# Performance work log

Measured on AMD Instinct MI355X. Metric: run time of the kernel, lower is better.

Reference implementation:

```python
import jax, jax.numpy as jnp
import numpy as np

EPS = 1e-5

def _conv3x3(x, w):
    # x: [B,C,H,W], w: [O,I,3,3], stride 1, padding 1
    return jax.lax.conv_general_dilated(
        x, w, window_strides=(1, 1), padding=((1, 1), (1, 1)),
        dimension_numbers=('NCHW', 'OIHW', 'NCHW'))

def _bn(x, gamma, beta, mean, var):
    inv = gamma / jnp.sqrt(var + EPS)
    return x * inv[None, :, None, None] + (beta - mean * inv)[None, :, None, None]

def setup_inputs() -> dict:
    key = jax.random.key(0)
    ks = jax.random.split(key, 6)
    B, C, H, W, E = 32, 64, 112, 112, 10
    x = jax.random.normal(ks[0], (B, C, H, W), dtype=jnp.float32)
    w1 = jax.random.normal(ks[1], (E, C, C, 3, 3), dtype=jnp.float32) * 0.05
    w2 = jax.random.normal(ks[2], (E, C, C, 3, 3), dtype=jnp.float32) * 0.05
    alpha = jax.random.uniform(ks[3], (E,), dtype=jnp.float32)
    return {
        'x': x, 'w1': w1, 'w2': w2, 'alpha': alpha,
        'bn1_gamma': jnp.ones((C,), jnp.float32),
        'bn1_beta': jnp.zeros((C,), jnp.float32),
        'bn1_mean': jnp.zeros((C,), jnp.float32),
        'bn1_var': jax.random.uniform(ks[4], (C,), jnp.float32) + 0.5,
        'bn2_gamma': jnp.ones((C,), jnp.float32),
        'bn2_beta': jnp.zeros((C,), jnp.float32),
        'bn2_mean': jnp.zeros((C,), jnp.float32),
        'bn2_var': jax.random.uniform(ks[5], (C,), jnp.float32) + 0.5,
    }

def reference(x, w1, w2, alpha,
              bn1_gamma, bn1_beta, bn1_mean, bn1_var,
              bn2_gamma, bn2_beta, bn2_mean, bn2_var):
    # Convolution is linear in its weights, so sum_i alpha[i] * conv(x, w_i)
    # == conv(x, sum_i alpha[i] * w_i): pre-combine experts into one kernel.
    w1_eff = jnp.einsum('e,eoihw->oihw', alpha, w1)
    w2_eff = jnp.einsum('e,eoihw->oihw', alpha, w2)
    out = _conv3x3(x, w1_eff)
    out = jax.nn.relu(_bn(out, bn1_gamma, bn1_beta, bn1_mean, bn1_var))
    out = _conv3x3(out, w2_eff)
    out = _bn(out, bn2_gamma, bn2_beta, bn2_mean, bn2_var)
    return jax.nn.relu(out + x)
```

## Files before the change

kernel.cpp:

```cpp
#include <hip/hip_runtime.h>


typedef __bf16 bf16x8 __attribute__((ext_vector_type(8)));
typedef float f32x4 __attribute__((ext_vector_type(4)));
typedef unsigned short u16;
typedef u16 u16x8 __attribute__((ext_vector_type(8)));

#define NH 112
#define NW 112
#define PH 114
#define PW 114
#define PROWB (PW * 128)
#define BUFB 23040
#define NTILES 3136

#define WAITVM(n) asm volatile("s_waitcnt vmcnt(" #n ")" ::: "memory")
#define SCHEDB __builtin_amdgcn_sched_barrier(0)

__device__ __forceinline__ u16 f2b(float f) {
  unsigned u = __builtin_bit_cast(unsigned, f);
  u += 0x7FFFu + ((u >> 16) & 1u);
  return (u16)(u >> 16);
}
__device__ __forceinline__ float b2f(u16 b) {
  unsigned u = ((unsigned)b) << 16;
  return __builtin_bit_cast(float, u);
}

__device__ __forceinline__ void gl_lds16(const void* g, void* l) {
  __builtin_amdgcn_global_load_lds(
      (const __attribute__((address_space(1))) unsigned int*)g,
      (__attribute__((address_space(3))) unsigned int*)l, 16, 0, 0);
}

__global__ void border_zero(u16* __restrict__ a, u16* __restrict__ bbuf) {
  int idx = blockIdx.x * 256 + threadIdx.x;
  if (idx >= 231424) return;
  int c8 = idx & 7;
  int t = idx >> 3;
  int buf = t >= 14464;
  t -= buf * 14464;
  int img = t / 452, e = t % 452;
  int h, w;
  if (e < 114) { h = 0; w = e; }
  else if (e < 228) { h = 113; w = e - 114; }
  else if (e < 340) { h = e - 227; w = 0; }
  else { h = e - 339; w = 113; }
  u16* base = buf ? bbuf : a;
  u16x8 z = {0, 0, 0, 0, 0, 0, 0, 0};
  *reinterpret_cast<u16x8*>(base + (((long)img * PH + h) * PW + w) * 64 + c8 * 8) = z;
}

__global__ __launch_bounds__(256) void transform_kernel(const float* __restrict__ x,
                                                        u16* __restrict__ xpad) {
  __shared__ alignas(16) u16 t[7168];
  int tid = threadIdx.x, bid = blockIdx.x;
  int b = bid / NH, h = bid % NH;
  const float* src = x + (long)b * 64 * 12544 + h * NW;
  f32x4 v[7];
#pragma unroll
  for (int it = 0; it < 7; ++it) {
    int fid = it * 256 + tid;
    int c = fid / 28, wq = fid % 28;
    v[it] = *reinterpret_cast<const f32x4*>(src + c * 12544 + wq * 4);
  }
#pragma unroll
  for (int it = 0; it < 7; ++it) {
    int fid = it * 256 + tid;
    int c = fid / 28, wq = fid % 28;
    int key = (wq & 7) << 4;
#pragma unroll
    for (int j = 0; j < 4; ++j) {
      int px = wq * 4 + j;
      *reinterpret_cast<u16*>((char*)t + px * 128 + ((c * 2) ^ key)) = f2b(v[it][j]);
    }
  }
  __syncthreads();
  int hp = h + 1;
  u16* rowb = xpad + (((long)b * PH + hp) * PW) * 64;
#pragma unroll
  for (int it = 0; it < 4; ++it) {
    int cidx = it * 256 + tid;
    if (cidx < 896) {
      int c8 = cidx & 7, px = cidx >> 3;
      int lchunk = c8 ^ ((px >> 2) & 7);
      u16x8 vv = *reinterpret_cast<const u16x8*>((const char*)t + px * 128 + lchunk * 16);
      int wp = px + 1;
      int gkey = (2 * hp + wp) & 7;
      *reinterpret_cast<u16x8*>(rowb + (long)wp * 64 + ((c8 ^ gkey) * 8)) = vv;
    }
  }
}

__global__ void prep_kernel(
    const float* __restrict__ w1, const float* __restrict__ w2,
    const float* __restrict__ alpha,
    const float* __restrict__ g1, const float* __restrict__ b1,
    const float* __restrict__ m1, const float* __restrict__ v1,
    const float* __restrict__ g2, const float* __restrict__ b2,
    const float* __restrict__ m2, const float* __restrict__ v2,
    u16* __restrict__ weff1, u16* __restrict__ weff2, float* __restrict__ bnc) {
  int idx = blockIdx.x * 256 + threadIdx.x;
  if (idx < 36864) {
    int i = idx & 63;
    int o = (idx >> 6) & 63;
    int kpos = idx >> 12;
    int base = (o * 64 + i) * 9 + kpos;
    float a1 = 0.f, a2 = 0.f;
#pragma unroll
    for (int e = 0; e < 10; ++e) {
      float al = alpha[e];
      a1 += al * w1[e * 36864 + base];
      a2 += al * w2[e * 36864 + base];
    }
    weff1[idx] = f2b(a1);
    weff2[idx] = f2b(a2);
  }
  if (blockIdx.x == 0 && threadIdx.x < 64) {
    int c = threadIdx.x;
    float i1 = g1[c] * rsqrtf(v1[c] + 1e-5f);
    float i2 = g2[c] * rsqrtf(v2[c] + 1e-5f);
    bnc[c] = i1;
    bnc[64 + c] = b1[c] - m1[c] * i1;
    bnc[128 + c] = i2;
    bnc[192 + c] = b2[c] - m2[c] * i2;
  }
}

__global__ __launch_bounds__(256, 2) void conv_p0_kernel(
    const u16* __restrict__ xin, const u16* __restrict__ weff,
    const float* __restrict__ bnc, u16* __restrict__ ypad) {
  __shared__ alignas(64) char smem[2 * BUFB];

  int tid = threadIdx.x, lane = tid & 63, wv = tid >> 6;
  int ol = lane & 15, kg = (lane >> 4) & 3;
  const int o = wv * 16 + ol;

  float inv = bnc[o];
  float bias = bnc[64 + o];

  bf16x8 wf[3][3][2];
#pragma unroll
  for (int kh = 0; kh < 3; ++kh)
#pragma unroll
    for (int kw = 0; kw < 3; ++kw)
#pragma unroll
      for (int ks = 0; ks < 2; ++ks)
        wf[kh][kw][ks] = __builtin_bit_cast(
            bf16x8, *reinterpret_cast<const u16x8*>(
                        weff + (((kh * 3 + kw) * 64 + o) * 64 + ks * 32 + kg * 8)));
  asm volatile("s_waitcnt vmcnt(0)" ::: "memory");
  SCHEDB;

  const int sb = (blockIdx.x & 7) * 64 + (blockIdx.x >> 3);
  const int n = (NTILES - sb + 511) >> 9;

  auto stage = [&](int tt, int boff) {
    int b = tt / 98;
    int r = tt % 98;
    int h0 = (r / 7) * 8, w0 = (r % 7) * 16;
    const char* src = (const char*)(xin + (((long)b * PH + h0) * PW + w0) * 64);
#pragma unroll
    for (int k = 0; k < 6; ++k) {
      int i = wv + k * 4;
      if (i < 23) {
        int cb = i * 64 + lane;
        if (cb < 1440) {
          int row = cb / 144, rem = cb % 144;
          gl_lds16(src + (long)row * PROWB + rem * 16, smem + boff + cb * 16);
        }
      }
    }
  };

  stage(sb, 0);
  asm volatile("" ::: "memory");
  stage(sb + 512, BUFB);
  asm volatile("" ::: "memory");
  if (wv < 3) WAITVM(6);
  else        WAITVM(5);
  SCHEDB;

  for (int j = 0; j < n; ++j) {
    const int boff = (j & 1) * BUFB;
    const int tt = sb + (j << 9);
    const int b = tt / 98;
    const int r = tt % 98;
    const int th0 = (r / 7) * 8, tw0 = (r % 7) * 16;

    __builtin_amdgcn_s_barrier();
    SCHEDB;

    f32x4 acc[8];
#pragma unroll
    for (int mf = 0; mf < 8; ++mf) acc[mf] = f32x4{0.f, 0.f, 0.f, 0.f};

#pragma unroll
    for (int kw = 0; kw < 3; ++kw)
#pragma unroll
      for (int ks = 0; ks < 2; ++ks) {
        const int col = ol + kw;
        const int sb8 = (ks << 2) | kg;
        bf16x8 a[4];
#pragma unroll
        for (int u = 0; u < 3; ++u) {
          int slot = sb8 ^ ((2 * u + col) & 7);
          a[u] = *reinterpret_cast<const bf16x8*>(smem + boff + (u * 18 + col) * 128 +
                                                  slot * 16);
        }
#pragma unroll
        for (int mf = 0; mf < 8; ++mf) {
          if (mf < 7) {
            int rr = mf + 3;
            int slot = sb8 ^ ((2 * rr + col) & 7);
            a[(mf + 3) & 3] = *reinterpret_cast<const bf16x8*>(
                smem + boff + (rr * 18 + col) * 128 + slot * 16);
          }
          acc[mf] = __builtin_amdgcn_mfma_f32_16x16x32_bf16(a[mf & 3], wf[0][kw][ks],
                                                            acc[mf], 0, 0, 0);
          acc[mf] = __builtin_amdgcn_mfma_f32_16x16x32_bf16(a[(mf + 1) & 3], wf[1][kw][ks],
                                                            acc[mf], 0, 0, 0);
          acc[mf] = __builtin_amdgcn_mfma_f32_16x16x32_bf16(a[(mf + 2) & 3], wf[2][kw][ks],
                                                            acc[mf], 0, 0, 0);
        }
      }

    SCHEDB;
    __builtin_amdgcn_s_barrier();
    SCHEDB;
    u16* ys = reinterpret_cast<u16*>(smem + boff);
#pragma unroll
    for (int mf = 0; mf < 8; ++mf)
#pragma unroll
      for (int rg = 0; rg < 4; ++rg) {
        int p = mf * 16 + kg * 4 + rg;
        ys[p * 72 + o] = f2b(fmaxf(acc[mf][rg] * inv + bias, 0.f));
      }
    asm volatile("s_waitcnt lgkmcnt(0)" ::: "memory");
    SCHEDB;
    __builtin_amdgcn_s_barrier();
    SCHEDB;
#pragma unroll
    for (int it = 0; it < 4; ++it) {
      int cidx = it * 256 + tid;
      int c8 = cidx & 7, p = cidx >> 3;
      int hp = th0 + (p >> 4) + 1, wp = tw0 + (p & 15) + 1;
      int gkey = (2 * hp + wp) & 7;
      *reinterpret_cast<u16x8*>(ypad + (((long)b * PH + hp) * PW + wp) * 64 +
                                ((c8 ^ gkey) * 8)) =
          *reinterpret_cast<const u16x8*>(ys + p * 72 + c8 * 8);
    }

    if (j + 1 < n) {
      SCHEDB;
      __builtin_amdgcn_s_barrier();
      SCHEDB;
      if (j + 2 < n) {
        stage(sb + ((j + 2) << 9), boff);
        if (wv < 3) WAITVM(6);
        else        WAITVM(5);
      } else {
        WAITVM(0);
      }
      SCHEDB;
    }
  }
}

template <int RESID>
__global__ __launch_bounds__(256, 2) void conv_p1_kernel(
    const u16* __restrict__ yin, const float* __restrict__ x,
    const u16* __restrict__ xres, const u16* __restrict__ weff,
    const float* __restrict__ bnc, float* __restrict__ out) {
  constexpr int BUF = RESID ? (BUFB + 16384) : BUFB;
  __shared__ alignas(64) char smem[2 * BUF];

  int tid = threadIdx.x, lane = tid & 63, wv = tid >> 6;
  int ol = lane & 15, kg = (lane >> 4) & 3;
  const int o = wv * 16 + ol;

  float inv = bnc[128 + o];
  float bias = bnc[192 + o];

  bf16x8 wf[3][3][2];
#pragma unroll
  for (int kh = 0; kh < 3; ++kh)
#pragma unroll
    for (int kw = 0; kw < 3; ++kw)
#pragma unroll
      for (int ks = 0; ks < 2; ++ks)
        wf[kh][kw][ks] = __builtin_bit_cast(
            bf16x8, *reinterpret_cast<const u16x8*>(
                        weff + (((kh * 3 + kw) * 64 + o) * 64 + ks * 32 + kg * 8)));
  asm volatile("s_waitcnt vmcnt(0)" ::: "memory");
  SCHEDB;

  const int sb = (blockIdx.x & 7) * 64 + (blockIdx.x >> 3);
  const int n = (NTILES - sb + 511) >> 9;

  auto stage = [&](int tt, int boff) {
    int b = tt / 98;
    int r = tt % 98;
    int h0 = (r / 7) * 8, w0 = (r % 7) * 16;
    const char* src = (const char*)(yin + (((long)b * PH + h0) * PW + w0) * 64);
#pragma unroll
    for (int k = 0; k < 6; ++k) {
      int i = wv + k * 4;
      if (i < 23) {
        int cb = i * 64 + lane;
        if (cb < 1440) {
          int row = cb / 144, rem = cb % 144;
          gl_lds16(src + (long)row * PROWB + rem * 16, smem + boff + cb * 16);
        }
      }
    }
    if constexpr (RESID) {
#pragma unroll
      for (int k = 0; k < 4; ++k) {
        int i = wv + k * 4;
        int cr = i * 64 + lane;
        int rp = cr >> 7, rem = cr & 127;
        gl_lds16((const char*)xres + (((long)b * PH + h0 + 1 + rp) * PW + w0 + 1) * 128 +
                     rem * 16,
                 smem + boff + BUFB + cr * 16);
      }
    }
  };
  auto gateS = [&] {
    if constexpr (RESID) {
      if (wv < 3) WAITVM(10); else WAITVM(9);
    } else {
      if (wv < 3) WAITVM(6); else WAITVM(5);
    }
  };

  stage(sb, 0);
  asm volatile("" ::: "memory");
  stage(sb + 512, BUF);
  asm volatile("" ::: "memory");
  gateS();
  SCHEDB;

  for (int j = 0; j < n; ++j) {
    const int boff = (j & 1) * BUF;
    const int tt = sb + (j << 9);
    const int b = tt / 98;
    const int r = tt % 98;
    const int th0 = (r / 7) * 8, tw0 = (r % 7) * 16;

    __builtin_amdgcn_s_barrier();
    SCHEDB;

    f32x4 acc[8];
#pragma unroll
    for (int mf = 0; mf < 8; ++mf) acc[mf] = f32x4{0.f, 0.f, 0.f, 0.f};

#pragma unroll
    for (int kw = 0; kw < 3; ++kw)
#pragma unroll
      for (int ks = 0; ks < 2; ++ks) {
        const int col = ol + kw;
        const int sb8 = (ks << 2) | kg;
        bf16x8 a[4];
#pragma unroll
        for (int u = 0; u < 3; ++u) {
          int slot = sb8 ^ ((2 * u + col) & 7);
          a[u] = *reinterpret_cast<const bf16x8*>(smem + boff + (u * 18 + col) * 128 +
                                                  slot * 16);
        }
#pragma unroll
        for (int mf = 0; mf < 8; ++mf) {
          if (mf < 7) {
            int rr = mf + 3;
            int slot = sb8 ^ ((2 * rr + col) & 7);
            a[(mf + 3) & 3] = *reinterpret_cast<const bf16x8*>(
                smem + boff + (rr * 18 + col) * 128 + slot * 16);
          }
          acc[mf] = __builtin_amdgcn_mfma_f32_16x16x32_bf16(a[mf & 3], wf[0][kw][ks],
                                                            acc[mf], 0, 0, 0);
          acc[mf] = __builtin_amdgcn_mfma_f32_16x16x32_bf16(a[(mf + 1) & 3], wf[1][kw][ks],
                                                            acc[mf], 0, 0, 0);
          acc[mf] = __builtin_amdgcn_mfma_f32_16x16x32_bf16(a[(mf + 2) & 3], wf[2][kw][ks],
                                                            acc[mf], 0, 0, 0);
        }
      }

    if constexpr (RESID) {
#pragma unroll
      for (int mf = 0; mf < 8; ++mf) {
        int h = th0 + mf, hp = h + 1;
        f32x4 vv;
#pragma unroll
        for (int rg = 0; rg < 4; ++rg) {
          int wq = kg * 4 + rg, wp = tw0 + wq + 1;
          int key = (2 * hp + wp) & 7;
          u16 bv = *reinterpret_cast<const u16*>(
              smem + boff + BUFB + (mf * 16 + wq) * 128 + (((o >> 3) ^ key) * 16) +
              (o & 7) * 2);
          vv[rg] = fmaxf(acc[mf][rg] * inv + bias + b2f(bv), 0.f);
        }
        *reinterpret_cast<f32x4*>(out + (((b * 64 + o) * NH + h) * NW + tw0 + kg * 4)) =
            vv;
      }
    } else {
#pragma unroll
      for (int half = 0; half < 2; ++half) {
        f32x4 xr[4];
#pragma unroll
        for (int m = 0; m < 4; ++m) {
          int h = th0 + half * 4 + m;
          xr[m] = *reinterpret_cast<const f32x4*>(
              x + (((b * 64 + o) * NH + h) * NW + tw0 + kg * 4));
        }
#pragma unroll
        for (int m = 0; m < 4; ++m) {
          int mf = half * 4 + m;
          int h = th0 + mf;
          f32x4 vv;
#pragma unroll
          for (int rg = 0; rg < 4; ++rg)
            vv[rg] = fmaxf(acc[mf][rg] * inv + bias + xr[m][rg], 0.f);
          *reinterpret_cast<f32x4*>(out + (((b * 64 + o) * NH + h) * NW + tw0 + kg * 4)) =
              vv;
        }
      }
    }

    if (j + 1 < n) {
      SCHEDB;
      __builtin_amdgcn_s_barrier();
      SCHEDB;
      if (j + 2 < n) {
        stage(sb + ((j + 2) << 9), boff);
        gateS();
      } else {
        WAITVM(0);
      }
      SCHEDB;
    }
  }
}

extern "C" void kernel_launch(void* const* d_in, const int* in_sizes, int n_in,
                              void* d_out, int out_size, void* d_ws, size_t ws_size,
                              hipStream_t stream) {
  const float* x = (const float*)d_in[0];
  const float* w1 = (const float*)d_in[1];
  const float* w2 = (const float*)d_in[2];
  const float* alpha = (const float*)d_in[3];
  const float* g1 = (const float*)d_in[4];
  const float* b1 = (const float*)d_in[5];
  const float* m1 = (const float*)d_in[6];
  const float* v1 = (const float*)d_in[7];
  const float* g2 = (const float*)d_in[8];
  const float* b2 = (const float*)d_in[9];
  const float* m2 = (const float*)d_in[10];
  const float* v2 = (const float*)d_in[11];
  float* out = (float*)d_out;

  char* ws = (char*)d_ws;
  u16* weff1 = (u16*)ws;
  u16* weff2 = (u16*)(ws + 73728);
  float* bnc = (float*)(ws + 147456);
  u16* y1pad = (u16*)(ws + 148480);
  const size_t PADB = 53231616ull;
  bool big = ws_size >= 148480ull + 2ull * PADB;
  u16* xpad = big ? (u16*)(ws + 148480 + PADB) : (u16*)d_out;

  border_zero<<<904, 256, 0, stream>>>(xpad, y1pad);
  transform_kernel<<<32 * NH, 256, 0, stream>>>(x, xpad);
  prep_kernel<<<144, 256, 0, stream>>>(w1, w2, alpha, g1, b1, m1, v1,
                                       g2, b2, m2, v2, weff1, weff2, bnc);
  conv_p0_kernel<<<512, 256, 0, stream>>>(xpad, weff1, bnc, y1pad);
  if (big)
    conv_p1_kernel<1><<<512, 256, 0, stream>>>(y1pad, x, xpad, weff2, bnc, out);
  else
    conv_p1_kernel<0><<<512, 256, 0, stream>>>(y1pad, x, nullptr, weff2, bnc, out);
}
```

Before: 119.5 us.

## Merge setup kernels, process two rows per transform block, widen conv_p0 grid

Merges border zeroing and weight/BN prep into one setup kernel, so one fewer kernel launch is needed. The transform kernel now handles two image rows per block, with a barrier between them, which halves its grid. conv_p0 goes from 512 to 632 blocks with a new tile stride, and it guards the second prefetch for blocks that have only one tile. The aim is to cut launch overhead and spread conv work over more of the device, at the cost of uneven tile counts per block.

```diff
diff --git a/kernel.cpp b/kernel.cpp
--- a/kernel.cpp
+++ b/kernel.cpp
@@ -33,66 +33,8 @@
       (__attribute__((address_space(3))) unsigned int*)l, 16, 0, 0);
 }
 
-__global__ void border_zero(u16* __restrict__ a, u16* __restrict__ bbuf) {
-  int idx = blockIdx.x * 256 + threadIdx.x;
-  if (idx >= 231424) return;
-  int c8 = idx & 7;
-  int t = idx >> 3;
-  int buf = t >= 14464;
-  t -= buf * 14464;
-  int img = t / 452, e = t % 452;
-  int h, w;
-  if (e < 114) { h = 0; w = e; }
-  else if (e < 228) { h = 113; w = e - 114; }
-  else if (e < 340) { h = e - 227; w = 0; }
-  else { h = e - 339; w = 113; }
-  u16* base = buf ? bbuf : a;
-  u16x8 z = {0, 0, 0, 0, 0, 0, 0, 0};
-  *reinterpret_cast<u16x8*>(base + (((long)img * PH + h) * PW + w) * 64 + c8 * 8) = z;
-}
-
-__global__ __launch_bounds__(256) void transform_kernel(const float* __restrict__ x,
-                                                        u16* __restrict__ xpad) {
-  __shared__ alignas(16) u16 t[7168];
-  int tid = threadIdx.x, bid = blockIdx.x;
-  int b = bid / NH, h = bid % NH;
-  const float* src = x + (long)b * 64 * 12544 + h * NW;
-  f32x4 v[7];
-#pragma unroll
-  for (int it = 0; it < 7; ++it) {
-    int fid = it * 256 + tid;
-    int c = fid / 28, wq = fid % 28;
-    v[it] = *reinterpret_cast<const f32x4*>(src + c * 12544 + wq * 4);
-  }
-#pragma unroll
-  for (int it = 0; it < 7; ++it) {
-    int fid = it * 256 + tid;
-    int c = fid / 28, wq = fid % 28;
-    int key = (wq & 7) << 4;
-#pragma unroll
-    for (int j = 0; j < 4; ++j) {
-      int px = wq * 4 + j;
-      *reinterpret_cast<u16*>((char*)t + px * 128 + ((c * 2) ^ key)) = f2b(v[it][j]);
-    }
-  }
-  __syncthreads();
-  int hp = h + 1;
-  u16* rowb = xpad + (((long)b * PH + hp) * PW) * 64;
-#pragma unroll
-  for (int it = 0; it < 4; ++it) {
-    int cidx = it * 256 + tid;
-    if (cidx < 896) {
-      int c8 = cidx & 7, px = cidx >> 3;
-      int lchunk = c8 ^ ((px >> 2) & 7);
-      u16x8 vv = *reinterpret_cast<const u16x8*>((const char*)t + px * 128 + lchunk * 16);
-      int wp = px + 1;
-      int gkey = (2 * hp + wp) & 7;
-      *reinterpret_cast<u16x8*>(rowb + (long)wp * 64 + ((c8 ^ gkey) * 8)) = vv;
-    }
-  }
-}
-
-__global__ void prep_kernel(
+__global__ void setup_kernel(
+    u16* __restrict__ a, u16* __restrict__ bbuf,
     const float* __restrict__ w1, const float* __restrict__ w2,
     const float* __restrict__ alpha,
     const float* __restrict__ g1, const float* __restrict__ b1,
@@ -100,7 +42,26 @@
     const float* __restrict__ g2, const float* __restrict__ b2,
     const float* __restrict__ m2, const float* __restrict__ v2,
     u16* __restrict__ weff1, u16* __restrict__ weff2, float* __restrict__ bnc) {
-  int idx = blockIdx.x * 256 + threadIdx.x;
+  int bid = blockIdx.x, tid = threadIdx.x;
+  if (bid < 904) {
+    int idx = bid * 256 + tid;
+    if (idx >= 231424) return;
+    int c8 = idx & 7;
+    int t = idx >> 3;
+    int buf = t >= 14464;
+    t -= buf * 14464;
+    int img = t / 452, e = t % 452;
+    int h, w;
+    if (e < 114) { h = 0; w = e; }
+    else if (e < 228) { h = 113; w = e - 114; }
+    else if (e < 340) { h = e - 227; w = 0; }
+    else { h = e - 339; w = 113; }
+    u16* base = buf ? bbuf : a;
+    u16x8 z = {0, 0, 0, 0, 0, 0, 0, 0};
+    *reinterpret_cast<u16x8*>(base + (((long)img * PH + h) * PW + w) * 64 + c8 * 8) = z;
+    return;
+  }
+  int idx = (bid - 904) * 256 + tid;
   if (idx < 36864) {
     int i = idx & 63;
     int o = (idx >> 6) & 63;
@@ -116,8 +77,8 @@
     weff1[idx] = f2b(a1);
     weff2[idx] = f2b(a2);
   }
-  if (blockIdx.x == 0 && threadIdx.x < 64) {
-    int c = threadIdx.x;
+  if (bid == 904 && tid < 64) {
+    int c = tid;
     float i1 = g1[c] * rsqrtf(v1[c] + 1e-5f);
     float i2 = g2[c] * rsqrtf(v2[c] + 1e-5f);
     bnc[c] = i1;
@@ -127,6 +88,53 @@
   }
 }
 
+__global__ __launch_bounds__(256) void transform_kernel(const float* __restrict__ x,
+                                                        u16* __restrict__ xpad) {
+  __shared__ alignas(16) u16 t[7168];
+  int tid = threadIdx.x;
+#pragma unroll
+  for (int jj = 0; jj < 2; ++jj) {
+    int bid = blockIdx.x * 2 + jj;
+    int b = bid / NH, h = bid % NH;
+    const float* src = x + (long)b * 64 * 12544 + h * NW;
+    f32x4 v[7];
+#pragma unroll
+    for (int it = 0; it < 7; ++it) {
+      int fid = it * 256 + tid;
+      int c = fid / 28, wq = fid % 28;
+      v[it] = *reinterpret_cast<const f32x4*>(src + c * 12544 + wq * 4);
+    }
+#pragma unroll
+    for (int it = 0; it < 7; ++it) {
+      int fid = it * 256 + tid;
+      int c = fid / 28, wq = fid % 28;
+      int key = (wq & 7) << 4;
+#pragma unroll
+      for (int j = 0; j < 4; ++j) {
+        int px = wq * 4 + j;
+        *reinterpret_cast<u16*>((char*)t + px * 128 + ((c * 2) ^ key)) = f2b(v[it][j]);
+      }
+    }
+    __syncthreads();
+    int hp = h + 1;
+    u16* rowb = xpad + (((long)b * PH + hp) * PW) * 64;
+#pragma unroll
+    for (int it = 0; it < 4; ++it) {
+      int cidx = it * 256 + tid;
+      if (cidx < 896) {
+        int c8 = cidx & 7, px = cidx >> 3;
+        int lchunk = c8 ^ ((px >> 2) & 7);
+        u16x8 vv =
+            *reinterpret_cast<const u16x8*>((const char*)t + px * 128 + lchunk * 16);
+        int wp = px + 1;
+        int gkey = (2 * hp + wp) & 7;
+        *reinterpret_cast<u16x8*>(rowb + (long)wp * 64 + ((c8 ^ gkey) * 8)) = vv;
+      }
+    }
+    if (jj == 0) __syncthreads();
+  }
+}
+
 __global__ __launch_bounds__(256, 2) void conv_p0_kernel(
     const u16* __restrict__ xin, const u16* __restrict__ weff,
     const float* __restrict__ bnc, u16* __restrict__ ypad) {
@@ -152,8 +160,8 @@
   asm volatile("s_waitcnt vmcnt(0)" ::: "memory");
   SCHEDB;
 
-  const int sb = (blockIdx.x & 7) * 64 + (blockIdx.x >> 3);
-  const int n = (NTILES - sb + 511) >> 9;
+  const int sb = (blockIdx.x & 7) * 79 + (blockIdx.x >> 3);
+  const int n = (NTILES - sb + 631) / 632;
 
   auto stage = [&](int tt, int boff) {
     int b = tt / 98;
@@ -175,15 +183,19 @@
 
   stage(sb, 0);
   asm volatile("" ::: "memory");
-  stage(sb + 512, BUFB);
+  if (n > 1) stage(sb + 632, BUFB);
   asm volatile("" ::: "memory");
-  if (wv < 3) WAITVM(6);
-  else        WAITVM(5);
+  if (n > 1) {
+    if (wv < 3) WAITVM(6);
+    else        WAITVM(5);
+  } else {
+    WAITVM(0);
+  }
   SCHEDB;
 
   for (int j = 0; j < n; ++j) {
     const int boff = (j & 1) * BUFB;
-    const int tt = sb + (j << 9);
+    const int tt = sb + j * 632;
     const int b = tt / 98;
     const int r = tt % 98;
     const int th0 = (r / 7) * 8, tw0 = (r % 7) * 16;
@@ -256,7 +268,7 @@
       __builtin_amdgcn_s_barrier();
       SCHEDB;
       if (j + 2 < n) {
-        stage(sb + ((j + 2) << 9), boff);
+        stage(sb + (j + 2) * 632, boff);
         if (wv < 3) WAITVM(6);
         else        WAITVM(5);
       } else {
@@ -467,11 +479,10 @@
   bool big = ws_size >= 148480ull + 2ull * PADB;
   u16* xpad = big ? (u16*)(ws + 148480 + PADB) : (u16*)d_out;
 
-  border_zero<<<904, 256, 0, stream>>>(xpad, y1pad);
-  transform_kernel<<<32 * NH, 256, 0, stream>>>(x, xpad);
-  prep_kernel<<<144, 256, 0, stream>>>(w1, w2, alpha, g1, b1, m1, v1,
-                                       g2, b2, m2, v2, weff1, weff2, bnc);
-  conv_p0_kernel<<<512, 256, 0, stream>>>(xpad, weff1, bnc, y1pad);
+  setup_kernel<<<1048, 256, 0, stream>>>(xpad, y1pad, w1, w2, alpha, g1, b1, m1,
+                                         v1, g2, b2, m2, v2, weff1, weff2, bnc);
+  transform_kernel<<<1792, 256, 0, stream>>>(x, xpad);
+  conv_p0_kernel<<<632, 256, 0, stream>>>(xpad, weff1, bnc, y1pad);
   if (big)
     conv_p1_kernel<1><<<512, 256, 0, stream>>>(y1pad, x, xpad, weff2, bnc, out);
   else
```

New measurement: 121.8 us. Within noise of the previous version (+2.0%).
